# Kernel optimization log

Measured on AMD Instinct MI355X. Metric: run time of the kernel, lower is better.

Reference implementation:

```python
import jax, jax.numpy as jnp
import numpy as np

N_NODES = 100000
N_EDGES = 1000000
D = 128          # input_dim == hidden_dim (required: h = zeros_like(nh) accumulates src_nf)
OUT = 128
NUM_TYPES = 5


def setup_inputs() -> dict:
    key = jax.random.key(0)
    ks = jax.random.split(key, 7)
    nh = jax.random.normal(ks[0], (N_NODES, D), dtype=jnp.float32)
    edge_y = jax.random.randint(ks[1], (N_EDGES,), 0, NUM_TYPES, dtype=jnp.int64)
    edge_index = jax.random.randint(ks[2], (2, N_EDGES), 0, N_NODES, dtype=jnp.int64)
    # nn.Linear weights, scaled for numerical sanity
    W_nf = jax.random.normal(ks[3], (D, D), dtype=jnp.float32) * 0.08
    W_attn = jax.random.normal(ks[4], (1, 2 * D), dtype=jnp.float32) * 0.08
    W_out = jax.random.normal(ks[5], (OUT, 2 * D), dtype=jnp.float32) * 0.08
    b_out = jax.random.normal(ks[6], (OUT,), dtype=jnp.float32) * 0.01
    return {"nh": nh, "edge_y": edge_y, "edge_index": edge_index,
            "W_nf": W_nf, "W_attn": W_attn, "W_out": W_out, "b_out": b_out}


def reference(nh, edge_y, edge_index, W_nf, W_attn, W_out, b_out):
    n = nh.shape[0]
    src, dst = edge_index[0], edge_index[1]

    # nf_lin applied once per node, then gathered per edge (same math as
    # self.nf_lin(nh[src]) since Linear is per-row)
    nfl = nh @ W_nf.T                                  # [N, D]
    src_nf = nfl[src]                                  # [E, D]
    dst_nf = nfl[dst]                                  # [E, D]

    # attn(cat([src_nf, dst_nf])) == src_nf @ a_src + dst_nf @ a_dst
    a_src, a_dst = W_attn[0, :D], W_attn[0, D:]
    ef = src_nf @ a_src + dst_nf @ a_dst               # [E]
    ef = jnp.where(ef >= 0, ef, 0.2 * ef)              # LeakyReLU(0.2)

    # scatter_softmax per (edge_type, dst) group: the per-type loop with
    # scatter_softmax over dst is exactly a segment softmax over composite
    # segments seg = dst*5 + type; the summed per-type scatter_adds equal
    # one segment_sum over dst.
    seg = dst * NUM_TYPES + edge_y                     # [E]
    num_seg = n * NUM_TYPES
    m = jax.ops.segment_max(ef, seg, num_segments=num_seg)
    ex = jnp.exp(ef - m[seg])
    denom = jax.ops.segment_sum(ex, seg, num_segments=num_seg)
    alpha = ex / denom[seg]                            # [E]

    h = jax.ops.segment_sum(alpha[:, None] * src_nf, dst, num_segments=n)  # [N, D]

    nf = jnp.concatenate([nh, h], axis=-1) @ W_out.T + b_out
    return jax.nn.relu(nf)
```

## Files before the change

kernel.cpp:

```cpp
#include <hip/hip_runtime.h>

#define NTYPES 5
#define EPB 16384
#define BKSH 6
#define BKDST 64
#define CAP 2048

typedef _Float16 half8 __attribute__((ext_vector_type(8)));
typedef _Float16 half4v __attribute__((ext_vector_type(4)));
typedef float float4v __attribute__((ext_vector_type(4)));

__device__ __forceinline__ void stage_f32(
    _Float16* lds, const float* __restrict__ g, int rows, int stride4, int off4,
    int grow0, int nmax, int t)
{
  const float4* g4 = (const float4*)g;
  for (int i = t; i < rows * 32; i += 256) {
    int row = i >> 5, q = i & 31;
    float4 v = make_float4(0.f, 0.f, 0.f, 0.f);
    int gr = grow0 + row;
    if (gr < nmax) v = g4[(size_t)gr * stride4 + off4 + q];
    half4v hv = { (_Float16)v.x, (_Float16)v.y, (_Float16)v.z, (_Float16)v.w };
    int byte = row * 256 + ((q * 8) ^ ((row & 7) << 4));
    *(half4v*)((char*)lds + byte) = hv;
  }
}

__device__ __forceinline__ half8 frag_ld(const _Float16* lds, int row, int khw) {
  int byte = row * 256 + ((khw * 2) ^ ((row & 7) << 4));
  return *(const half8*)((const char*)lds + byte);
}

__device__ __forceinline__ half8 cvt8(float4 v0, float4 v1) {
  half8 a;
  a[0] = (_Float16)v0.x; a[1] = (_Float16)v0.y; a[2] = (_Float16)v0.z; a[3] = (_Float16)v0.w;
  a[4] = (_Float16)v1.x; a[5] = (_Float16)v1.y; a[6] = (_Float16)v1.z; a[7] = (_Float16)v1.w;
  return a;
}

struct A8 { float4 v[8]; };
__device__ __forceinline__ A8 loadA8(const float* __restrict__ nh, int arow, int n, int g) {
  A8 r;
  const float4* p = (const float4*)(nh + (size_t)arow * 128);
  bool ok = arow < n;
  float4 z = make_float4(0.f, 0.f, 0.f, 0.f);
  #pragma unroll
  for (int s = 0; s < 4; ++s) {
    r.v[2 * s]     = ok ? p[s * 8 + g * 2]     : z;
    r.v[2 * s + 1] = ok ? p[s * 8 + g * 2 + 1] : z;
  }
  return r;
}

__global__ __launch_bounds__(256) void k_gemm0(
    const float* __restrict__ nh, const float* __restrict__ Wnf,
    const float* __restrict__ Wattn,
    float* __restrict__ s_src, float* __restrict__ s_dst,
    _Float16* __restrict__ nfl, _Float16* __restrict__ nh16, int n)
{
  __shared__ _Float16 wh[128 * 128];
  const int t = threadIdx.x, lane = t & 63, wv = t >> 6;
  const int r16 = lane & 15, g = lane >> 4;
  stage_f32(wh, Wnf, 128, 32, 0, 0, 1 << 30, t);
  float asrc[8], adst[8];
  #pragma unroll
  for (int nf = 0; nf < 8; ++nf) {
    asrc[nf] = Wattn[nf * 16 + r16];
    adst[nf] = Wattn[128 + nf * 16 + r16];
  }
  __syncthreads();
  const int nchunk = (n + 63) >> 6;
  const int gstride = gridDim.x;
  int c = blockIdx.x;
  A8 cur;
  if (c < nchunk) cur = loadA8(nh, (c << 6) + wv * 16 + r16, n, g);
  for (; c < nchunk; c += gstride) {
    const int base = c << 6;
    int cn = c + gstride;
    A8 nxt;
    #pragma unroll
    for (int q = 0; q < 8; ++q) nxt.v[q] = make_float4(0.f, 0.f, 0.f, 0.f);
    if (cn < nchunk) nxt = loadA8(nh, (cn << 6) + wv * 16 + r16, n, g);

    const int arow = base + wv * 16 + r16;
    float4v acc[8];
    #pragma unroll
    for (int nf = 0; nf < 8; ++nf) acc[nf] = (float4v){0.f, 0.f, 0.f, 0.f};
    #pragma unroll
    for (int s = 0; s < 4; ++s) {
      half8 a = cvt8(cur.v[2 * s], cur.v[2 * s + 1]);
      if (arow < n) *(half8*)(nh16 + (size_t)arow * 128 + s * 32 + g * 8) = a;
      #pragma unroll
      for (int nf = 0; nf < 8; ++nf)
        acc[nf] = __builtin_amdgcn_mfma_f32_16x16x32_f16(a, frag_ld(wh, nf * 16 + r16, s * 32 + g * 8), acc[nf], 0, 0, 0);
    }
    #pragma unroll
    for (int rr = 0; rr < 4; ++rr) {
      int node = base + wv * 16 + g * 4 + rr;
      if (node >= n) continue;
      size_t ro = (size_t)node * 128;
      #pragma unroll
      for (int nf = 0; nf < 8; ++nf) nfl[ro + nf * 16 + r16] = (_Float16)acc[nf][rr];
    }
    float ss[4] = {0.f, 0.f, 0.f, 0.f}, sd[4] = {0.f, 0.f, 0.f, 0.f};
    #pragma unroll
    for (int nf = 0; nf < 8; ++nf)
      #pragma unroll
      for (int rr = 0; rr < 4; ++rr) {
        ss[rr] = fmaf(acc[nf][rr], asrc[nf], ss[rr]);
        sd[rr] = fmaf(acc[nf][rr], adst[nf], sd[rr]);
      }
    #pragma unroll
    for (int m = 1; m <= 8; m <<= 1)
      #pragma unroll
      for (int rr = 0; rr < 4; ++rr) {
        ss[rr] += __shfl_xor(ss[rr], m);
        sd[rr] += __shfl_xor(sd[rr], m);
      }
    if (r16 == 0) {
      #pragma unroll
      for (int rr = 0; rr < 4; ++rr) {
        int node = base + wv * 16 + g * 4 + rr;
        if (node < n) { s_src[node] = ss[rr]; s_dst[node] = sd[rr]; }
      }
    }
    cur = nxt;
  }
}

__global__ __launch_bounds__(256) void k_hist(
    const int* __restrict__ dsts, int* __restrict__ cnt, int e, int nbk, int nblk)
{
  __shared__ int hist[2048];
  const int t = threadIdx.x, b = blockIdx.x;
  for (int k = t; k < nbk; k += 256) hist[k] = 0;
  __syncthreads();
  const int i0 = b * EPB;
  const int iend = min(i0 + EPB, e);
  for (int i = i0 + t; i < iend; i += 256)
    atomicAdd(&hist[dsts[i] >> BKSH], 1);
  __syncthreads();
  for (int k = t; k < nbk; k += 256) cnt[k * nblk + b] = hist[k];
}

__global__ __launch_bounds__(256) void k_scan1(
    const int* __restrict__ deg, int* __restrict__ base, int* __restrict__ bsum, int n)
{
  __shared__ int ws[4];
  int t = threadIdx.x;
  int g0 = blockIdx.x * 1024 + t * 4;
  int4 v = make_int4(0, 0, 0, 0);
  if (g0 + 3 < n) v = *(const int4*)(deg + g0);
  else {
    if (g0     < n) v.x = deg[g0];
    if (g0 + 1 < n) v.y = deg[g0 + 1];
    if (g0 + 2 < n) v.z = deg[g0 + 2];
    if (g0 + 3 < n) v.w = deg[g0 + 3];
  }
  int s = v.x + v.y + v.z + v.w;
  int inc = s;
  #pragma unroll
  for (int d = 1; d < 64; d <<= 1) {
    int o = __shfl_up(inc, d);
    if ((t & 63) >= d) inc += o;
  }
  int wid = t >> 6;
  if ((t & 63) == 63) ws[wid] = inc;
  __syncthreads();
  int woff = 0;
  for (int w = 0; w < wid; ++w) woff += ws[w];
  int exc = woff + inc - s;
  if (g0 + 3 < n) {
    *(int4*)(base + g0) = make_int4(exc, exc + v.x, exc + v.x + v.y, exc + v.x + v.y + v.z);
  } else {
    if (g0     < n) base[g0]     = exc;
    if (g0 + 1 < n) base[g0 + 1] = exc + v.x;
    if (g0 + 2 < n) base[g0 + 2] = exc + v.x + v.y;
  }
  if (t == 255) bsum[blockIdx.x] = woff + inc;
}

__global__ __launch_bounds__(256) void k_scan2(
    const int* __restrict__ bsum, int* __restrict__ boff, int nb)
{
  __shared__ int ws[4];
  int t = threadIdx.x;
  int x = t < nb ? bsum[t] : 0;
  int inc = x;
  #pragma unroll
  for (int d = 1; d < 64; d <<= 1) {
    int o = __shfl_up(inc, d);
    if ((t & 63) >= d) inc += o;
  }
  int wid = t >> 6;
  if ((t & 63) == 63) ws[wid] = inc;
  __syncthreads();
  int woff = 0;
  for (int w = 0; w < wid; ++w) woff += ws[w];
  if (t < nb) boff[t] = woff + inc - x;
}

__global__ __launch_bounds__(256) void k_scan3(
    int* __restrict__ base, const int* __restrict__ boff, int n)
{
  int i = blockIdx.x * 256 + threadIdx.x;
  if (i < n) base[i] += boff[i >> 10];
}

__global__ __launch_bounds__(256) void k_scatter2(
    const int* __restrict__ ei, const int* __restrict__ ey,
    const int* __restrict__ cnt_s, unsigned* __restrict__ rec,
    int e, int nbk, int nblk)
{
  __shared__ int cur[2048];
  const int t = threadIdx.x, b = blockIdx.x;
  for (int k = t; k < nbk; k += 256) cur[k] = cnt_s[k * nblk + b];
  __syncthreads();
  const int i0 = b * EPB;
  const int iend = min(i0 + EPB, e);
  for (int i = i0 + t; i < iend; i += 256) {
    int s = ei[i], d = ei[e + i], ty = ey[i];
    int pos = atomicAdd(&cur[d >> BKSH], 1);
    rec[pos] = (unsigned)s | ((unsigned)ty << 17) | ((unsigned)(d & (BKDST - 1)) << 20);
  }
}

__global__ __launch_bounds__(256) void k_agg2(
    const unsigned* __restrict__ rec, const int* __restrict__ cnt_s,
    const float* __restrict__ s_src, const float* __restrict__ s_dst,
    const _Float16* __restrict__ nfl, _Float16* __restrict__ h,
    int n, int e, int nbk, int nblk)
{
  __shared__ unsigned ord[CAP];
  __shared__ float efl[CAP];
  __shared__ int dcnt[BKDST];
  __shared__ int dbase[BKDST + 1];
  __shared__ float sdl[BKDST];
  const int t = threadIdx.x;
  const int k = blockIdx.x;
  const int d0 = k << BKSH;
  const int ndst = min(BKDST, n - d0);
  const int bs = cnt_s[k * nblk];
  const int be = (k + 1 < nbk) ? cnt_s[(k + 1) * nblk] : e;
  const int cnt = be - bs;
  if (t < BKDST) {
    dcnt[t] = 0;
    if (t < ndst) sdl[t] = s_dst[d0 + t];
  }
  __syncthreads();
  const int g = t >> 4, l = t & 15;

  if (cnt <= CAP) {
    for (int i = t; i < cnt; i += 256)
      atomicAdd(&dcnt[(rec[bs + i] >> 20) & (BKDST - 1)], 1);
    __syncthreads();
    if (t < BKDST) {
      int v = dcnt[t];
      int inc = v;
      #pragma unroll
      for (int dd = 1; dd < 64; dd <<= 1) {
        int o = __shfl_up(inc, dd);
        if (t >= dd) inc += o;
      }
      dbase[t] = inc - v;
      dcnt[t]  = inc - v;
      if (t == BKDST - 1) dbase[BKDST] = inc;
    }
    __syncthreads();
    for (int i = t; i < cnt; i += 256) {
      unsigned p = rec[bs + i];
      int pos = atomicAdd(&dcnt[(p >> 20) & (BKDST - 1)], 1);
      ord[pos] = p;
    }
    __syncthreads();
    for (int i = t; i < cnt; i += 256) {
      unsigned p = ord[i];
      float ef = s_src[p & 0x1FFFF] + sdl[(p >> 20) & (BKDST - 1)];
      efl[i] = ef >= 0.f ? ef : 0.2f * ef;
    }
    __syncthreads();
    for (int di = g; di < ndst; di += 16) {
      int s0 = dbase[di], deg = dbase[di + 1] - s0;
      float acc[8] = {0.f, 0.f, 0.f, 0.f, 0.f, 0.f, 0.f, 0.f};
      if (deg > 0) {
        float mx[NTYPES];
        #pragma unroll
        for (int tt = 0; tt < NTYPES; ++tt) mx[tt] = -1e30f;
        for (int j0 = 0; j0 < deg; j0 += 16) {
          int jj = j0 + l;
          bool ok = jj < deg;
          float ef = ok ? efl[s0 + jj] : -1e30f;
          int ty = ok ? (int)((ord[s0 + jj] >> 17) & 7) : 7;
          #pragma unroll
          for (int tt = 0; tt < NTYPES; ++tt) {
            float v = (ty == tt) ? ef : -1e30f;
            v = fmaxf(v, __shfl_xor(v, 1)); v = fmaxf(v, __shfl_xor(v, 2));
            v = fmaxf(v, __shfl_xor(v, 4)); v = fmaxf(v, __shfl_xor(v, 8));
            mx[tt] = fmaxf(mx[tt], v);
          }
        }
        float sm[NTYPES];
        #pragma unroll
        for (int tt = 0; tt < NTYPES; ++tt) sm[tt] = 0.f;
        for (int j0 = 0; j0 < deg; j0 += 16) {
          int jj = j0 + l;
          bool ok = jj < deg;
          int ty = ok ? (int)((ord[s0 + jj] >> 17) & 7) : 7;
          float ex = ok ? __expf(efl[s0 + jj] - mx[ty]) : 0.f;
          if (ok) efl[s0 + jj] = ex;
          #pragma unroll
          for (int tt = 0; tt < NTYPES; ++tt) {
            float v = (ty == tt) ? ex : 0.f;
            v += __shfl_xor(v, 1); v += __shfl_xor(v, 2);
            v += __shfl_xor(v, 4); v += __shfl_xor(v, 8);
            sm[tt] += v;
          }
        }
        float rsm[NTYPES];
        #pragma unroll
        for (int tt = 0; tt < NTYPES; ++tt) rsm[tt] = sm[tt] > 0.f ? 1.f / sm[tt] : 0.f;
        int j = 0;
        for (; j + 4 <= deg; j += 4) {
          unsigned p0 = ord[s0 + j],     p1 = ord[s0 + j + 1];
          unsigned p2 = ord[s0 + j + 2], p3 = ord[s0 + j + 3];
          float a0 = efl[s0 + j]     * rsm[(p0 >> 17) & 7];
          float a1 = efl[s0 + j + 1] * rsm[(p1 >> 17) & 7];
          float a2 = efl[s0 + j + 2] * rsm[(p2 >> 17) & 7];
          float a3 = efl[s0 + j + 3] * rsm[(p3 >> 17) & 7];
          half8 x0 = *(const half8*)(nfl + (size_t)(p0 & 0x1FFFF) * 128 + l * 8);
          half8 x1 = *(const half8*)(nfl + (size_t)(p1 & 0x1FFFF) * 128 + l * 8);
          half8 x2 = *(const half8*)(nfl + (size_t)(p2 & 0x1FFFF) * 128 + l * 8);
          half8 x3 = *(const half8*)(nfl + (size_t)(p3 & 0x1FFFF) * 128 + l * 8);
          #pragma unroll
          for (int kk = 0; kk < 8; ++kk) acc[kk] = fmaf(a0, (float)x0[kk], acc[kk]);
          #pragma unroll
          for (int kk = 0; kk < 8; ++kk) acc[kk] = fmaf(a1, (float)x1[kk], acc[kk]);
          #pragma unroll
          for (int kk = 0; kk < 8; ++kk) acc[kk] = fmaf(a2, (float)x2[kk], acc[kk]);
          #pragma unroll
          for (int kk = 0; kk < 8; ++kk) acc[kk] = fmaf(a3, (float)x3[kk], acc[kk]);
        }
        for (; j < deg; ++j) {
          unsigned p0 = ord[s0 + j];
          float a0 = efl[s0 + j] * rsm[(p0 >> 17) & 7];
          half8 x0 = *(const half8*)(nfl + (size_t)(p0 & 0x1FFFF) * 128 + l * 8);
          #pragma unroll
          for (int kk = 0; kk < 8; ++kk) acc[kk] = fmaf(a0, (float)x0[kk], acc[kk]);
        }
      }
      half8 hv;
      #pragma unroll
      for (int kk = 0; kk < 8; ++kk) hv[kk] = (_Float16)acc[kk];
      *(half8*)(h + (size_t)(d0 + di) * 128 + l * 8) = hv;
    }
  } else {
    const int gb = (t & 63) & 48;
    for (int di = g; di < ndst; di += 16) {
      float mx[NTYPES], sm[NTYPES];
      #pragma unroll
      for (int tt = 0; tt < NTYPES; ++tt) { mx[tt] = -1e30f; sm[tt] = 0.f; }
      for (int j0 = 0; j0 < cnt; j0 += 16) {
        int jj = j0 + l;
        unsigned p = (jj < cnt) ? rec[bs + jj] : 0xFFFFFFFFu;
        bool mine = (p != 0xFFFFFFFFu) && (int)((p >> 20) & (BKDST - 1)) == di;
        float ef = -1e30f; int ty = 7;
        if (mine) {
          ef = s_src[p & 0x1FFFF] + sdl[di];
          ef = ef >= 0.f ? ef : 0.2f * ef;
          ty = (p >> 17) & 7;
        }
        #pragma unroll
        for (int tt = 0; tt < NTYPES; ++tt) {
          float v = (mine && ty == tt) ? ef : -1e30f;
          v = fmaxf(v, __shfl_xor(v, 1)); v = fmaxf(v, __shfl_xor(v, 2));
          v = fmaxf(v, __shfl_xor(v, 4)); v = fmaxf(v, __shfl_xor(v, 8));
          mx[tt] = fmaxf(mx[tt], v);
        }
      }
      for (int j0 = 0; j0 < cnt; j0 += 16) {
        int jj = j0 + l;
        unsigned p = (jj < cnt) ? rec[bs + jj] : 0xFFFFFFFFu;
        bool mine = (p != 0xFFFFFFFFu) && (int)((p >> 20) & (BKDST - 1)) == di;
        float ex = 0.f; int ty = 7;
        if (mine) {
          float ef = s_src[p & 0x1FFFF] + sdl[di];
          ef = ef >= 0.f ? ef : 0.2f * ef;
          ty = (p >> 17) & 7;
          ex = __expf(ef - mx[ty]);
        }
        #pragma unroll
        for (int tt = 0; tt < NTYPES; ++tt) {
          float v = (ty == tt) ? ex : 0.f;
          v += __shfl_xor(v, 1); v += __shfl_xor(v, 2);
          v += __shfl_xor(v, 4); v += __shfl_xor(v, 8);
          sm[tt] += v;
        }
      }
      float rsm[NTYPES];
      #pragma unroll
      for (int tt = 0; tt < NTYPES; ++tt) rsm[tt] = sm[tt] > 0.f ? 1.f / sm[tt] : 0.f;
      float acc[8] = {0.f, 0.f, 0.f, 0.f, 0.f, 0.f, 0.f, 0.f};
      for (int j0 = 0; j0 < cnt; j0 += 16) {
        int jj = j0 + l;
        unsigned p = (jj < cnt) ? rec[bs + jj] : 0xFFFFFFFFu;
        bool mine = (p != 0xFFFFFFFFu) && (int)((p >> 20) & (BKDST - 1)) == di;
        float al = 0.f;
        if (mine) {
          float ef = s_src[p & 0x1FFFF] + sdl[di];
          ef = ef >= 0.f ? ef : 0.2f * ef;
          int ty = (p >> 17) & 7;
          al = __expf(ef - mx[ty]) * rsm[ty];
        }
        unsigned pv = mine ? p : 0xFFFFFFFFu;
        for (int jj2 = 0; jj2 < 16; ++jj2) {
          unsigned pp = __shfl(pv, gb + jj2);
          float aa = __shfl(al, gb + jj2);
          if (pp != 0xFFFFFFFFu) {
            half8 x = *(const half8*)(nfl + (size_t)(pp & 0x1FFFF) * 128 + l * 8);
            #pragma unroll
            for (int kk = 0; kk < 8; ++kk) acc[kk] = fmaf(aa, (float)x[kk], acc[kk]);
          }
        }
      }
      half8 hv;
      #pragma unroll
      for (int kk = 0; kk < 8; ++kk) hv[kk] = (_Float16)acc[kk];
      *(half8*)(h + (size_t)(d0 + di) * 128 + l * 8) = hv;
    }
  }
}

__global__ __launch_bounds__(256) void k_gemmO(
    const _Float16* __restrict__ nh16, const _Float16* __restrict__ hbuf,
    const float* __restrict__ Wout, const float* __restrict__ bias,
    float* __restrict__ out, int n)
{
  __shared__ _Float16 w1[64 * 128], w2[64 * 128];
  const int t = threadIdx.x, lane = t & 63, wv = t >> 6;
  const int r16 = lane & 15, g = lane >> 4;
  const int jhalf = blockIdx.x & 1;
  stage_f32(w1, Wout, 64, 64, 0,  jhalf * 64, 1 << 30, t);
  stage_f32(w2, Wout, 64, 64, 32, jhalf * 64, 1 << 30, t);
  float bv[4];
  #pragma unroll
  for (int nf = 0; nf < 4; ++nf) bv[nf] = bias[jhalf * 64 + nf * 16 + r16];
  __syncthreads();
  const int nchunk = (n + 63) >> 6;
  const int gstride = gridDim.x >> 1;
  int c = blockIdx.x >> 1;
  half8 c1[4], c2[4];
  if (c < nchunk) {
    int arow = (c << 6) + wv * 16 + r16;
    bool ok = arow < n;
    #pragma unroll
    for (int s = 0; s < 4; ++s) {
      c1[s] = ok ? *(const half8*)(nh16 + (size_t)arow * 128 + s * 32 + g * 8) : (half8){};
      c2[s] = ok ? *(const half8*)(hbuf + (size_t)arow * 128 + s * 32 + g * 8) : (half8){};
    }
  }
  for (; c < nchunk; c += gstride) {
    const int base = c << 6;
    int cn = c + gstride;
    half8 n1[4] = {}, n2[4] = {};
    if (cn < nchunk) {
      int arow = (cn << 6) + wv * 16 + r16;
      bool ok = arow < n;
      #pragma unroll
      for (int s = 0; s < 4; ++s) {
        n1[s] = ok ? *(const half8*)(nh16 + (size_t)arow * 128 + s * 32 + g * 8) : (half8){};
        n2[s] = ok ? *(const half8*)(hbuf + (size_t)arow * 128 + s * 32 + g * 8) : (half8){};
      }
    }
    float4v acc[4];
    #pragma unroll
    for (int nf = 0; nf < 4; ++nf) acc[nf] = (float4v){0.f, 0.f, 0.f, 0.f};
    #pragma unroll
    for (int s = 0; s < 4; ++s) {
      #pragma unroll
      for (int nf = 0; nf < 4; ++nf) {
        acc[nf] = __builtin_amdgcn_mfma_f32_16x16x32_f16(c1[s], frag_ld(w1, nf * 16 + r16, s * 32 + g * 8), acc[nf], 0, 0, 0);
        acc[nf] = __builtin_amdgcn_mfma_f32_16x16x32_f16(c2[s], frag_ld(w2, nf * 16 + r16, s * 32 + g * 8), acc[nf], 0, 0, 0);
      }
    }
    #pragma unroll
    for (int rr = 0; rr < 4; ++rr) {
      int node = base + wv * 16 + g * 4 + rr;
      if (node >= n) continue;
      #pragma unroll
      for (int nf = 0; nf < 4; ++nf)
        out[(size_t)node * 128 + jhalf * 64 + nf * 16 + r16] = fmaxf(acc[nf][rr] + bv[nf], 0.f);
    }
    #pragma unroll
    for (int s = 0; s < 4; ++s) { c1[s] = n1[s]; c2[s] = n2[s]; }
  }
}

extern "C" void kernel_launch(void* const* d_in, const int* in_sizes, int n_in,
                              void* d_out, int out_size, void* d_ws, size_t ws_size,
                              hipStream_t stream) {
  const float* nh     = (const float*)d_in[0];
  const int*   edge_y = (const int*)d_in[1];
  const int*   ei     = (const int*)d_in[2];
  const float* W_nf   = (const float*)d_in[3];
  const float* W_attn = (const float*)d_in[4];
  const float* W_out  = (const float*)d_in[5];
  const float* b_out  = (const float*)d_in[6];
  float* out = (float*)d_out;
  const int n = in_sizes[0] / 128;
  const int e = in_sizes[1];
  const int nbk  = (n + BKDST - 1) >> BKSH;
  const int nblk = (e + EPB - 1) / EPB;
  const int ncnt = nbk * nblk;
  const int nb2  = (ncnt + 1023) / 1024;

  _Float16* nfl_h = (_Float16*)d_ws;
  _Float16* nh16  = nfl_h + (size_t)n * 128;
  _Float16* h_h   = nh16 + (size_t)n * 128;
  float* s_src = (float*)(h_h + (size_t)n * 128);
  float* s_dst = s_src + n;
  int*   cnt   = (int*)(s_dst + n);
  int*   bsum  = cnt + ncnt;
  int*   boff  = bsum + 256;
  unsigned* rec = (unsigned*)(boff + 256);

  k_gemm0<<<1280, 256, 0, stream>>>(nh, W_nf, W_attn, s_src, s_dst, nfl_h, nh16, n);
  k_hist<<<nblk, 256, 0, stream>>>(ei + e, cnt, e, nbk, nblk);
  k_scan1<<<nb2, 256, 0, stream>>>(cnt, cnt, bsum, ncnt);
  k_scan2<<<1, 256, 0, stream>>>(bsum, boff, nb2);
  k_scan3<<<(ncnt + 255) / 256, 256, 0, stream>>>(cnt, boff, ncnt);
  k_scatter2<<<nblk, 256, 0, stream>>>(ei, edge_y, cnt, rec, e, nbk, nblk);
  k_agg2<<<nbk, 256, 0, stream>>>(rec, cnt, s_src, s_dst, nfl_h, h_h, n, e, nbk, nblk);
  k_gemmO<<<1280, 256, 0, stream>>>(nh16, h_h, W_out, b_out, out, n);
}
```

Baseline: 192.9 us.

## Halve destination bucket size and drop register prefetch in node GEMM

Destination buckets shrink from 64 to 32 nodes (CAP 1024), so the per-bucket local sort and aggregation work on smaller groups and more blocks are launched. The shared histogram arrays in the histogram and scatter kernels grow to 4096 entries to hold the doubled bucket count. The node GEMM kernel drops its software prefetch of the next chunk's input rows and loads the current chunk directly. This lowers register pressure but exposes load latency. The loading code also contains a redundant first load loop whose values are immediately overwritten.

```diff
diff --git a/kernel.cpp b/kernel.cpp
--- a/kernel.cpp
+++ b/kernel.cpp
@@ -2,9 +2,9 @@
 
 #define NTYPES 5
 #define EPB 16384
-#define BKSH 6
-#define BKDST 64
-#define CAP 2048
+#define BKSH 5
+#define BKDST 32
+#define CAP 1024
 
 typedef _Float16 half8 __attribute__((ext_vector_type(8)));
 typedef _Float16 half4v __attribute__((ext_vector_type(4)));
@@ -38,20 +38,6 @@
   return a;
 }
 
-struct A8 { float4 v[8]; };
-__device__ __forceinline__ A8 loadA8(const float* __restrict__ nh, int arow, int n, int g) {
-  A8 r;
-  const float4* p = (const float4*)(nh + (size_t)arow * 128);
-  bool ok = arow < n;
-  float4 z = make_float4(0.f, 0.f, 0.f, 0.f);
-  #pragma unroll
-  for (int s = 0; s < 4; ++s) {
-    r.v[2 * s]     = ok ? p[s * 8 + g * 2]     : z;
-    r.v[2 * s + 1] = ok ? p[s * 8 + g * 2 + 1] : z;
-  }
-  return r;
-}
-
 __global__ __launch_bounds__(256) void k_gemm0(
     const float* __restrict__ nh, const float* __restrict__ Wnf,
     const float* __restrict__ Wattn,
@@ -70,26 +56,27 @@
   }
   __syncthreads();
   const int nchunk = (n + 63) >> 6;
-  const int gstride = gridDim.x;
-  int c = blockIdx.x;
-  A8 cur;
-  if (c < nchunk) cur = loadA8(nh, (c << 6) + wv * 16 + r16, n, g);
-  for (; c < nchunk; c += gstride) {
+  for (int c = blockIdx.x; c < nchunk; c += gridDim.x) {
     const int base = c << 6;
-    int cn = c + gstride;
-    A8 nxt;
-    #pragma unroll
-    for (int q = 0; q < 8; ++q) nxt.v[q] = make_float4(0.f, 0.f, 0.f, 0.f);
-    if (cn < nchunk) nxt = loadA8(nh, (cn << 6) + wv * 16 + r16, n, g);
-
     const int arow = base + wv * 16 + r16;
+    const bool ok = arow < n;
+    const float4* nh4 = (const float4*)(nh + (size_t)arow * 128);
+    float4 av[8];
+    const float4 z = make_float4(0.f, 0.f, 0.f, 0.f);
+    #pragma unroll
+    for (int q = 0; q < 8; ++q) av[q] = ok ? nh4[q * 4 + g * 2 - (q & 1) * (g * 2) + 0] : z;
+    #pragma unroll
+    for (int s = 0; s < 4; ++s) {
+      av[2 * s]     = ok ? nh4[s * 8 + g * 2]     : z;
+      av[2 * s + 1] = ok ? nh4[s * 8 + g * 2 + 1] : z;
+    }
     float4v acc[8];
     #pragma unroll
     for (int nf = 0; nf < 8; ++nf) acc[nf] = (float4v){0.f, 0.f, 0.f, 0.f};
     #pragma unroll
     for (int s = 0; s < 4; ++s) {
-      half8 a = cvt8(cur.v[2 * s], cur.v[2 * s + 1]);
-      if (arow < n) *(half8*)(nh16 + (size_t)arow * 128 + s * 32 + g * 8) = a;
+      half8 a = cvt8(av[2 * s], av[2 * s + 1]);
+      if (ok) *(half8*)(nh16 + (size_t)arow * 128 + s * 32 + g * 8) = a;
       #pragma unroll
       for (int nf = 0; nf < 8; ++nf)
         acc[nf] = __builtin_amdgcn_mfma_f32_16x16x32_f16(a, frag_ld(wh, nf * 16 + r16, s * 32 + g * 8), acc[nf], 0, 0, 0);
@@ -124,14 +111,13 @@
         if (node < n) { s_src[node] = ss[rr]; s_dst[node] = sd[rr]; }
       }
     }
-    cur = nxt;
   }
 }
 
 __global__ __launch_bounds__(256) void k_hist(
     const int* __restrict__ dsts, int* __restrict__ cnt, int e, int nbk, int nblk)
 {
-  __shared__ int hist[2048];
+  __shared__ int hist[4096];
   const int t = threadIdx.x, b = blockIdx.x;
   for (int k = t; k < nbk; k += 256) hist[k] = 0;
   __syncthreads();
@@ -212,7 +198,7 @@
     const int* __restrict__ cnt_s, unsigned* __restrict__ rec,
     int e, int nbk, int nblk)
 {
-  __shared__ int cur[2048];
+  __shared__ int cur[4096];
   const int t = threadIdx.x, b = blockIdx.x;
   for (int k = t; k < nbk; k += 256) cur[k] = cnt_s[k * nblk + b];
   __syncthreads();
@@ -258,7 +244,7 @@
       int v = dcnt[t];
       int inc = v;
       #pragma unroll
-      for (int dd = 1; dd < 64; dd <<= 1) {
+      for (int dd = 1; dd < BKDST; dd <<= 1) {
         int o = __shfl_up(inc, dd);
         if (t >= dd) inc += o;
       }
```

After: 181.4 us. 5.9% less time.
